# Kernel optimization log

Hardware: AMD Instinct MI355X
Metric: run time of the kernel (lower is better)

The kernel has to match this reference:

```python
import jax, jax.numpy as jnp
import numpy as np
import itertools

KS = 5           # kernel_size per pseudo dim
PDIM = 2         # pseudo-coordinate dim
N_NODES = 50000
N_EDGES = 800000
D_IN = 128
D_OUT = 128
EPS = 1e-12


def l2norm(x):
    n = jnp.linalg.norm(x, axis=-1, keepdims=True)
    return x / jnp.maximum(n, EPS)


def spline_conv(x, src, dst, pseudo, weight, bias):
    """torch_spline_conv with degree=1, open splines, aggr='mean', no root weight."""
    N = x.shape[0]
    out_dim = weight.shape[-1]
    dim = pseudo.shape[1]
    v = pseudo * (KS - 1)                                   # [E, dim] in [0, KS-1)
    i0 = jnp.clip(jnp.floor(v), 0, KS - 2).astype(jnp.int32)
    frac = v - i0.astype(v.dtype)                           # [E, dim]
    # Precompute per-kernel transforms once per node: cheaper than per-edge GEMV
    Xk = jnp.einsum('ni,kio->nko', x, weight)               # [N, K=25, out]
    E = src.shape[0]
    y = jnp.zeros((E, out_dim), x.dtype)
    for bits in itertools.product((0, 1), repeat=dim):      # S = 2**dim = 4 combos
        b = jnp.ones((E,), x.dtype)
        wi = jnp.zeros((E,), jnp.int32)
        stride = 1
        for d, bit in enumerate(bits):
            b = b * (frac[:, d] if bit else 1.0 - frac[:, d])
            wi = wi + (i0[:, d] + bit) * stride
            stride *= KS
        y = y + b[:, None] * Xk[src, wi]                    # gather-weight per edge
    agg = jax.ops.segment_sum(y, dst, num_segments=N)       # scatter-add to targets
    deg = jax.ops.segment_sum(jnp.ones((E,), x.dtype), dst, num_segments=N)
    return agg / jnp.maximum(deg, 1.0)[:, None] + bias      # mean aggregation


def setup_inputs() -> dict:
    key = jax.random.key(0)
    ks = jax.random.split(key, 6)
    K = KS ** PDIM
    x = jax.random.normal(ks[0], (N_NODES, D_IN), jnp.float32)
    edge_index = jax.random.randint(ks[1], (2, N_EDGES), 0, N_NODES, jnp.int32)
    edge_attr = jax.random.uniform(ks[2], (N_EDGES, PDIM), jnp.float32)
    s0 = 1.0 / np.sqrt(K * D_IN)
    s1 = 1.0 / np.sqrt(K * D_OUT)
    w0 = jax.random.normal(ks[3], (K, D_IN, D_OUT), jnp.float32) * s0
    w1 = jax.random.normal(ks[4], (K, D_OUT, D_OUT), jnp.float32) * s1
    b0 = jnp.zeros((D_OUT,), jnp.float32)
    b1 = jnp.zeros((D_OUT,), jnp.float32)
    return {"x": x, "edge_index": edge_index, "edge_attr": edge_attr,
            "w0": w0, "b0": b0, "w1": w1, "b1": b1}


def reference(x, edge_index, edge_attr, w0, b0, w1, b1):
    src, dst = edge_index[0], edge_index[1]
    xs = [l2norm(x)]
    h = x
    for w, b in ((w0, b0), (w1, b1)):
        h = spline_conv(h, src, dst, edge_attr, w, b)
        xs.append(l2norm(h))
        h = jax.nn.relu(h)
    return jnp.concatenate(xs, axis=-1)                     # [N, D_IN + 2*D_OUT]
```

## Files before the change

### kernel.cpp

```cpp
#include <hip/hip_runtime.h>

#define D     128
#define OD    384
#define NK    25
#define KCMAX 13
#define KB0   13

typedef __attribute__((ext_vector_type(8))) short bf16x8;
typedef __attribute__((ext_vector_type(4))) float f32x4;
typedef __attribute__((ext_vector_type(4))) unsigned int u32x4;
typedef const __attribute__((address_space(1))) void gv_t;
typedef __attribute__((address_space(3))) void lv_t;

struct __align__(16) Rec {
  int src;
  unsigned int wi;
  unsigned int b01;
  unsigned int b23;
};

__device__ inline unsigned short f2bf(float f) {
  unsigned int u = __float_as_uint(f);
  u += 0x7fffu + ((u >> 16) & 1u);
  return (unsigned short)(u >> 16);
}
__device__ inline unsigned short f2h(float f) {
  return __builtin_bit_cast(unsigned short, (_Float16)f);
}
__device__ inline float h2f(unsigned int bits16) {
  return (float)__builtin_bit_cast(_Float16, (unsigned short)(bits16 & 0xffffu));
}


__device__ inline int edge_cls(int w00) {
  return (w00 + 6 < KB0) ? 0 : ((w00 >= KB0) ? 2 : 1);
}

__global__ __launch_bounds__(256) void count3_kernel(const int* __restrict__ dstA,
    const float* __restrict__ attr, int E, int* __restrict__ deg,
    int* __restrict__ cnt3) {
  int e = blockIdx.x * 256 + threadIdx.x;
  if (e >= E) return;
  int d = dstA[e];
  atomicAdd(&deg[d], 1);
  float v0 = attr[2 * e] * 4.0f;
  float v1 = attr[2 * e + 1] * 4.0f;
  int i0 = min(3, max(0, (int)v0));
  int i1 = min(3, max(0, (int)v1));
  int w00 = i0 + 5 * i1;
  atomicAdd(&cnt3[d * 3 + edge_cls(w00)], 1);
}


__global__ __launch_bounds__(1024) void scan_a_kernel(const int* __restrict__ cnt, int M,
    int* __restrict__ base3, int* __restrict__ bsum) {
  __shared__ int tmp[1024];
  int tid = threadIdx.x;
  int e = blockIdx.x * 1024 + tid;
  int v = (e < M) ? cnt[e] : 0;
  tmp[tid] = v;
  __syncthreads();
#pragma unroll
  for (int off = 1; off < 1024; off <<= 1) {
    int t = (tid >= off) ? tmp[tid - off] : 0;
    __syncthreads();
    tmp[tid] += t;
    __syncthreads();
  }
  if (e <= M) base3[e] = tmp[tid] - v;
  if (tid == 1023) bsum[blockIdx.x] = tmp[1023];
}

__global__ __launch_bounds__(256) void scan_b_kernel(int* __restrict__ bsum, int nblk) {
  __shared__ int tmp[256];
  __shared__ int carry;
  int tid = threadIdx.x;
  if (tid == 0) carry = 0;
  __syncthreads();
  for (int s = 0; s < nblk; s += 256) {
    int i = s + tid;
    int v = (i < nblk) ? bsum[i] : 0;
    tmp[tid] = v;
    __syncthreads();
#pragma unroll
    for (int off = 1; off < 256; off <<= 1) {
      int t = (tid >= off) ? tmp[tid - off] : 0;
      __syncthreads();
      tmp[tid] += t;
      __syncthreads();
    }
    if (i < nblk) bsum[i] = carry + tmp[tid] - v;
    __syncthreads();
    if (tid == 255) carry += tmp[255];
    __syncthreads();
  }
}

__global__ __launch_bounds__(256) void scan_c_kernel(int* __restrict__ base3,
    int* __restrict__ cursor, const int* __restrict__ bsum, int M) {
  int e = blockIdx.x * 256 + threadIdx.x;
  if (e > M) return;
  int v = base3[e] + bsum[e >> 10];
  base3[e] = v;
  if (e < M) cursor[e] = v;
}

__global__ __launch_bounds__(256) void fill_kernel(const int* __restrict__ srcA,
    const int* __restrict__ dstA, const float* __restrict__ attr, int E,
    int* __restrict__ cursor, Rec* __restrict__ recs) {
  int e = blockIdx.x * 256 + threadIdx.x;
  if (e >= E) return;
  int d = dstA[e];
  float v0 = attr[2 * e] * 4.0f;
  float v1 = attr[2 * e + 1] * 4.0f;
  int i0 = min(3, max(0, (int)v0));
  int i1 = min(3, max(0, (int)v1));
  float f0 = v0 - (float)i0;
  float f1 = v1 - (float)i1;
  int w00 = i0 + 5 * i1;
  int pos = atomicAdd(&cursor[d * 3 + edge_cls(w00)], 1);
  Rec r;
  r.src = srcA[e];
  unsigned int w = (unsigned int)w00;
  r.wi = w | ((w + 1) << 5) | ((w + 5) << 10) | ((w + 6) << 15);
  r.b01 = (unsigned int)f2h((1.f - f0) * (1.f - f1)) | ((unsigned int)f2h(f0 * (1.f - f1)) << 16);
  r.b23 = (unsigned int)f2h((1.f - f0) * f1) | ((unsigned int)f2h(f0 * f1) << 16);
  recs[pos] = r;
}

__global__ __launch_bounds__(256) void wt_kernel(const float* __restrict__ W,
                                                 unsigned short* __restrict__ WT) {
  int idx = blockIdx.x * 256 + threadIdx.x;
  if (idx >= 128 * NK * D) return;
  int n = idx / (NK * D);
  int kk = idx - n * (NK * D);
  WT[idx] = f2bf(W[(size_t)kk * D + n]);
}


__global__ __launch_bounds__(256) void gather_kernel(const int* __restrict__ base3,
    const Rec* __restrict__ recs, const unsigned short* __restrict__ Xb,
    unsigned short* __restrict__ Gc, int N, int KCc, int kc0, int c_lo, int c_hi) {
  __shared__ float lacc[4][KCMAX * D];
  int w = threadIdx.x >> 6, l = threadIdx.x & 63;
  int dst = blockIdx.x * 4 + w;
  if (dst >= N) return;
  float* A = lacc[w];
  for (int k = 0; k < KCc; ++k)
    *(float2*)(A + k * D + l * 2) = make_float2(0.f, 0.f);

  auto ACC = [&](const Rec& r, unsigned int xp) {
    float x0 = __uint_as_float(xp << 16);
    float x1 = __uint_as_float(xp & 0xffff0000u);
    float bq[4] = {h2f(r.b01), h2f(r.b01 >> 16), h2f(r.b23), h2f(r.b23 >> 16)};
#pragma unroll
    for (int q = 0; q < 4; ++q) {
      int k = (int)((r.wi >> (5 * q)) & 31u) - kc0;
      if ((unsigned)k < (unsigned)KCc) {
        float2 p = *(const float2*)(A + k * D + l * 2);
        p.x = fmaf(bq[q], x0, p.x);
        p.y = fmaf(bq[q], x1, p.y);
        *(float2*)(A + k * D + l * 2) = p;
      }
    }
  };

  int s = __builtin_amdgcn_readfirstlane(base3[dst * 3 + c_lo]);
  int e = __builtin_amdgcn_readfirstlane(base3[dst * 3 + c_hi]);
  int j = s;
  for (; j + 3 < e; j += 4) {
    Rec r0 = recs[j], r1 = recs[j + 1], r2 = recs[j + 2], r3 = recs[j + 3];
    unsigned int xp0 = *(const unsigned int*)(Xb + (size_t)r0.src * D + l * 2);
    unsigned int xp1 = *(const unsigned int*)(Xb + (size_t)r1.src * D + l * 2);
    unsigned int xp2 = *(const unsigned int*)(Xb + (size_t)r2.src * D + l * 2);
    unsigned int xp3 = *(const unsigned int*)(Xb + (size_t)r3.src * D + l * 2);
    ACC(r0, xp0); ACC(r1, xp1); ACC(r2, xp2); ACC(r3, xp3);
  }
  for (; j < e; ++j) {
    Rec r = recs[j];
    unsigned int xp = *(const unsigned int*)(Xb + (size_t)r.src * D + l * 2);
    ACC(r, xp);
  }

  unsigned short* gr = Gc + (size_t)dst * ((size_t)KCc * D);
  for (int t = l; t < KCc * 16; t += 64) {
    const float* src = A + (t >> 4) * D + (t & 15) * 8;
    float4 v0 = *(const float4*)(src);
    float4 v1 = *(const float4*)(src + 4);
    u32x4 pk;
    pk[0] = (unsigned int)f2bf(v0.x) | ((unsigned int)f2bf(v0.y) << 16);
    pk[1] = (unsigned int)f2bf(v0.z) | ((unsigned int)f2bf(v0.w) << 16);
    pk[2] = (unsigned int)f2bf(v1.x) | ((unsigned int)f2bf(v1.y) << 16);
    pk[3] = (unsigned int)f2bf(v1.z) | ((unsigned int)f2bf(v1.w) << 16);
    *(u32x4*)(gr + (size_t)t * 8) = pk;
  }
}


__global__ __launch_bounds__(256) void gemm_kernel(
    const unsigned short* __restrict__ G, const unsigned short* __restrict__ WT,
    float* __restrict__ Y, int N, int KCc, int kc0, int first) {
  __shared__ __attribute__((aligned(16))) char At[2][16384];
  __shared__ __attribute__((aligned(16))) char Bt[2][16384];
  const int tid = threadIdx.x;
  const int w = tid >> 6;
  const int l = tid & 63;
  const int m0 = blockIdx.x * 128;
  const size_t ldG = (size_t)KCc * 256;
  const size_t ldW = (size_t)NK * 256;

  const int lrow = l >> 3;
  const int scol = ((l & 7) * 16) ^ (lrow << 4);

  f32x4 acc[2][8];
#pragma unroll
  for (int mr = 0; mr < 2; ++mr)
#pragma unroll
    for (int nc = 0; nc < 8; ++nc) {
      if (first) {
        acc[mr][nc] = (f32x4){0.f, 0.f, 0.f, 0.f};
      } else {
        int col = nc * 16 + (l & 15);
#pragma unroll
        for (int j = 0; j < 4; ++j) {
          int row = m0 + w * 32 + mr * 16 + (l >> 4) * 4 + j;
          acc[mr][nc][j] = (row < N) ? Y[(size_t)row * D + col] : 0.f;
        }
      }
    }

  const int steps = KCc * 2;
  auto STAGE = [&](int kt, int b) {
#pragma unroll
    for (int i = 0; i < 4; ++i) {
      int row = w * 32 + i * 8 + lrow;
      int node = m0 + row;
      if (node > N - 1) node = N - 1;
      const char* src = (const char*)G + (size_t)node * ldG + kt * 128 + scol;
      __builtin_amdgcn_global_load_lds((gv_t*)src, (lv_t*)(At[b] + (w * 4 + i) * 1024),
                                       16, 0, 0);
    }
#pragma unroll
    for (int i = 0; i < 4; ++i) {
      int nr = w * 32 + i * 8 + lrow;
      const char* src = (const char*)WT + (size_t)nr * ldW + kc0 * 256 + kt * 128 + scol;
      __builtin_amdgcn_global_load_lds((gv_t*)src, (lv_t*)(Bt[b] + (w * 4 + i) * 1024),
                                       16, 0, 0);
    }
  };

  STAGE(0, 0);
  __syncthreads();
  for (int kt = 0; kt < steps; ++kt) {
    const int cur = kt & 1;
    if (kt + 1 < steps) STAGE(kt + 1, cur ^ 1);
#pragma unroll
    for (int ks = 0; ks < 2; ++ks) {
      int kb = ks * 64 + (l >> 4) * 16;
      bf16x8 a[2], b[8];
#pragma unroll
      for (int mr = 0; mr < 2; ++mr) {
        int r = w * 32 + mr * 16 + (l & 15);
        a[mr] = *(const bf16x8*)(At[cur] + r * 128 + (kb ^ ((r & 7) << 4)));
      }
#pragma unroll
      for (int nc = 0; nc < 8; ++nc) {
        int nr = nc * 16 + (l & 15);
        b[nc] = *(const bf16x8*)(Bt[cur] + nr * 128 + (kb ^ ((nr & 7) << 4)));
      }
#pragma unroll
      for (int mr = 0; mr < 2; ++mr)
#pragma unroll
        for (int nc = 0; nc < 8; ++nc)
          acc[mr][nc] =
              __builtin_amdgcn_mfma_f32_16x16x32_bf16(a[mr], b[nc], acc[mr][nc], 0, 0, 0);
    }
    __syncthreads();
  }

#pragma unroll
  for (int mr = 0; mr < 2; ++mr)
#pragma unroll
    for (int nc = 0; nc < 8; ++nc) {
      int col = nc * 16 + (l & 15);
#pragma unroll
      for (int j = 0; j < 4; ++j) {
        int row = m0 + w * 32 + mr * 16 + (l >> 4) * 4 + j;
        if (row < N) Y[(size_t)row * D + col] = acc[mr][nc][j];
      }
    }
}


__global__ __launch_bounds__(256) void l2norm_x_kernel(const float* __restrict__ x,
    float* __restrict__ out, unsigned short* __restrict__ xbf, int N) {
  int g = blockIdx.x * 256 + threadIdx.x;
  int n = g >> 6, lane = g & 63;
  if (n >= N) return;
  float2 v = *(const float2*)(x + (size_t)n * D + lane * 2);
  float ss = v.x * v.x + v.y * v.y;
#pragma unroll
  for (int m = 1; m < 64; m <<= 1) ss += __shfl_xor(ss, m, 64);
  float r = 1.0f / fmaxf(sqrtf(ss), 1e-12f);
  *(float2*)(out + (size_t)n * OD + lane * 2) = make_float2(v.x * r, v.y * r);
  unsigned int pk = (unsigned int)f2bf(v.x) | ((unsigned int)f2bf(v.y) << 16);
  *(unsigned int*)(xbf + (size_t)n * D + lane * 2) = pk;
}

__global__ __launch_bounds__(256) void finalize_kernel(const float* __restrict__ y,
    const int* __restrict__ deg, const float* __restrict__ bias, float* __restrict__ out,
    unsigned short* __restrict__ xnext, int N) {
  int g = blockIdx.x * 256 + threadIdx.x;
  int n = g >> 6, lane = g & 63;
  if (n >= N) return;
  float inv = 1.0f / (float)max(deg[n], 1);
  float2 a = *(const float2*)(y + (size_t)n * D + lane * 2);
  float2 b = *(const float2*)(bias + lane * 2);
  float h0 = a.x * inv + b.x;
  float h1 = a.y * inv + b.y;
  float ss = h0 * h0 + h1 * h1;
#pragma unroll
  for (int m = 1; m < 64; m <<= 1) ss += __shfl_xor(ss, m, 64);
  float r = 1.0f / fmaxf(sqrtf(ss), 1e-12f);
  *(float2*)(out + (size_t)n * OD + lane * 2) = make_float2(h0 * r, h1 * r);
  if (xnext) {
    unsigned int pk = (unsigned int)f2bf(fmaxf(h0, 0.f)) |
                      ((unsigned int)f2bf(fmaxf(h1, 0.f)) << 16);
    *(unsigned int*)(xnext + (size_t)n * D + lane * 2) = pk;
  }
}


extern "C" void kernel_launch(void* const* d_in, const int* in_sizes, int n_in,
                              void* d_out, int out_size, void* d_ws, size_t ws_size,
                              hipStream_t stream) {
  const float* x    = (const float*)d_in[0];
  const int*   ei   = (const int*)d_in[1];
  const float* attr = (const float*)d_in[2];
  const float* w0   = (const float*)d_in[3];
  const float* b0   = (const float*)d_in[4];
  const float* w1   = (const float*)d_in[5];
  const float* b1   = (const float*)d_in[6];
  float* out = (float*)d_out;

  const int N = in_sizes[0] / D;
  const int E = in_sizes[1] / 2;
  const int* srcA = ei;
  const int* dstA = ei + E;
  const int M3 = N * 3;

  char* p = (char*)d_ws;
  auto carve = [&](size_t bytes) -> char* {
    char* r = p;
    p += (bytes + 255) & ~(size_t)255;
    return r;
  };
  unsigned short* xbf    = (unsigned short*)carve((size_t)N * D * 2);
  unsigned short* xtmp   = (unsigned short*)carve((size_t)N * D * 2);
  float*          ygemm  = (float*)carve((size_t)N * D * 4);
  int*            deg    = (int*)carve((size_t)N * 4);
  int*            cnt3   = (int*)carve((size_t)M3 * 4);
  int*            base3  = (int*)carve(((size_t)M3 + 1) * 4);
  int*            cursor = (int*)carve((size_t)M3 * 4);
  int*            bsum   = (int*)carve(4096);
  Rec*            recs   = (Rec*)carve((size_t)E * sizeof(Rec));
  unsigned short* WT0    = (unsigned short*)carve((size_t)128 * NK * D * 2);
  unsigned short* WT1    = (unsigned short*)carve((size_t)128 * NK * D * 2);
  size_t used = (size_t)(p - (char*)d_ws);
  size_t remain = (ws_size > used) ? (ws_size - used) : 0;
  int KCg = (int)(remain / ((size_t)N * D * 2));
  if (KCg > KCMAX) KCg = KCMAX;
  if (KCg < 1) KCg = 1;
  unsigned short* Gc = (unsigned short*)carve((size_t)N * (size_t)KCg * D * 2);
  (void)n_in; (void)out_size;

  hipMemsetAsync(deg, 0, (size_t)N * 4, stream);
  hipMemsetAsync(cnt3, 0, (size_t)M3 * 4, stream);

  int eb = (E + 255) / 256;
  count3_kernel<<<eb, 256, 0, stream>>>(dstA, attr, E, deg, cnt3);
  int nblk_a = (M3 + 1 + 1023) / 1024;
  scan_a_kernel<<<nblk_a, 1024, 0, stream>>>(cnt3, M3, base3, bsum);
  scan_b_kernel<<<1, 256, 0, stream>>>(bsum, nblk_a);
  scan_c_kernel<<<(M3 + 1 + 255) / 256, 256, 0, stream>>>(base3, cursor, bsum, M3);
  fill_kernel<<<eb, 256, 0, stream>>>(srcA, dstA, attr, E, cursor, recs);
  int wtb = (128 * NK * D + 255) / 256;
  wt_kernel<<<wtb, 256, 0, stream>>>(w0, WT0);
  wt_kernel<<<wtb, 256, 0, stream>>>(w1, WT1);

  int nb = (N * 64 + 255) / 256;
  l2norm_x_kernel<<<nb, 256, 0, stream>>>(x, out, xbf, N);

  int gbg = (N + 3) / 4;
  int gbm = (N + 127) / 128;
  const unsigned short* xin = xbf;
  const float* Bv[2] = {b0, b1};
  const unsigned short* WTl[2] = {WT0, WT1};
  for (int layer = 0; layer < 2; ++layer) {
    if (KCg >= KB0) {
      gather_kernel<<<gbg, 256, 0, stream>>>(base3, recs, xin, Gc, N, KB0, 0, 0, 2);
      gemm_kernel<<<gbm, 256, 0, stream>>>(Gc, WTl[layer], ygemm, N, KB0, 0, 1);
      gather_kernel<<<gbg, 256, 0, stream>>>(base3, recs, xin, Gc, N, NK - KB0, KB0, 1, 3);
      gemm_kernel<<<gbm, 256, 0, stream>>>(Gc, WTl[layer], ygemm, N, NK - KB0, KB0, 0);
    } else {
      int first = 1;
      for (int kc0 = 0; kc0 < NK; kc0 += KCg) {
        int KCc = min(KCg, NK - kc0);
        gather_kernel<<<gbg, 256, 0, stream>>>(base3, recs, xin, Gc, N, KCc, kc0, 0, 3);
        gemm_kernel<<<gbm, 256, 0, stream>>>(Gc, WTl[layer], ygemm, N, KCc, kc0, first);
        first = 0;
      }
    }
    finalize_kernel<<<nb, 256, 0, stream>>>(ygemm, deg, Bv[layer], out + D * (layer + 1),
                                            layer == 0 ? xtmp : nullptr, N);
    xin = xtmp;
  }
}
```

Baseline: 640.8 us.

## Fuse gather and GEMM per kernel-row chunk, bucketing edges by row index

```diff
diff --git a/kernel.cpp b/kernel.cpp
--- a/kernel.cpp
+++ b/kernel.cpp
@@ -1,20 +1,18 @@
 #include <hip/hip_runtime.h>
 
-#define D     128
-#define OD    384
-#define NK    25
-#define KCMAX 13
-#define KB0   13
+#define D    128
+#define OD   384
+#define NK   25
+#define KC   5
+#define AST  132
 
 typedef __attribute__((ext_vector_type(8))) short bf16x8;
 typedef __attribute__((ext_vector_type(4))) float f32x4;
 typedef __attribute__((ext_vector_type(4))) unsigned int u32x4;
-typedef const __attribute__((address_space(1))) void gv_t;
-typedef __attribute__((address_space(3))) void lv_t;
 
 struct __align__(16) Rec {
   int src;
-  unsigned int wi;
+  int i0;
   unsigned int b01;
   unsigned int b23;
 };
@@ -32,28 +30,20 @@
 }
 
 
-__device__ inline int edge_cls(int w00) {
-  return (w00 + 6 < KB0) ? 0 : ((w00 >= KB0) ? 2 : 1);
-}
-
-__global__ __launch_bounds__(256) void count3_kernel(const int* __restrict__ dstA,
+__global__ __launch_bounds__(256) void count4_kernel(const int* __restrict__ dstA,
     const float* __restrict__ attr, int E, int* __restrict__ deg,
-    int* __restrict__ cnt3) {
+    int* __restrict__ cnt4) {
   int e = blockIdx.x * 256 + threadIdx.x;
   if (e >= E) return;
   int d = dstA[e];
   atomicAdd(&deg[d], 1);
-  float v0 = attr[2 * e] * 4.0f;
   float v1 = attr[2 * e + 1] * 4.0f;
-  int i0 = min(3, max(0, (int)v0));
   int i1 = min(3, max(0, (int)v1));
-  int w00 = i0 + 5 * i1;
-  atomicAdd(&cnt3[d * 3 + edge_cls(w00)], 1);
-}
-
+  atomicAdd(&cnt4[d * 4 + i1], 1);
+}
 
 __global__ __launch_bounds__(1024) void scan_a_kernel(const int* __restrict__ cnt, int M,
-    int* __restrict__ base3, int* __restrict__ bsum) {
+    int* __restrict__ base, int* __restrict__ bsum) {
   __shared__ int tmp[1024];
   int tid = threadIdx.x;
   int e = blockIdx.x * 1024 + tid;
@@ -67,7 +57,7 @@
     tmp[tid] += t;
     __syncthreads();
   }
-  if (e <= M) base3[e] = tmp[tid] - v;
+  if (e <= M) base[e] = tmp[tid] - v;
   if (tid == 1023) bsum[blockIdx.x] = tmp[1023];
 }
 
@@ -96,12 +86,12 @@
   }
 }
 
-__global__ __launch_bounds__(256) void scan_c_kernel(int* __restrict__ base3,
+__global__ __launch_bounds__(256) void scan_c_kernel(int* __restrict__ base,
     int* __restrict__ cursor, const int* __restrict__ bsum, int M) {
   int e = blockIdx.x * 256 + threadIdx.x;
   if (e > M) return;
-  int v = base3[e] + bsum[e >> 10];
-  base3[e] = v;
+  int v = base[e] + bsum[e >> 10];
+  base[e] = v;
   if (e < M) cursor[e] = v;
 }
 
@@ -117,13 +107,12 @@
   int i1 = min(3, max(0, (int)v1));
   float f0 = v0 - (float)i0;
   float f1 = v1 - (float)i1;
-  int w00 = i0 + 5 * i1;
-  int pos = atomicAdd(&cursor[d * 3 + edge_cls(w00)], 1);
+  int pos = atomicAdd(&cursor[d * 4 + i1], 1);
   Rec r;
   r.src = srcA[e];
-  unsigned int w = (unsigned int)w00;
-  r.wi = w | ((w + 1) << 5) | ((w + 5) << 10) | ((w + 6) << 15);
-  r.b01 = (unsigned int)f2h((1.f - f0) * (1.f - f1)) | ((unsigned int)f2h(f0 * (1.f - f1)) << 16);
+  r.i0 = i0;
+  r.b01 = (unsigned int)f2h((1.f - f0) * (1.f - f1)) |
+          ((unsigned int)f2h(f0 * (1.f - f1)) << 16);
   r.b23 = (unsigned int)f2h((1.f - f0) * f1) | ((unsigned int)f2h(f0 * f1) << 16);
   recs[pos] = r;
 }
@@ -138,157 +127,99 @@
 }
 
 
-__global__ __launch_bounds__(256) void gather_kernel(const int* __restrict__ base3,
-    const Rec* __restrict__ recs, const unsigned short* __restrict__ Xb,
-    unsigned short* __restrict__ Gc, int N, int KCc, int kc0, int c_lo, int c_hi) {
-  __shared__ float lacc[4][KCMAX * D];
-  int w = threadIdx.x >> 6, l = threadIdx.x & 63;
-  int dst = blockIdx.x * 4 + w;
-  if (dst >= N) return;
-  float* A = lacc[w];
-  for (int k = 0; k < KCc; ++k)
-    *(float2*)(A + k * D + l * 2) = make_float2(0.f, 0.f);
-
-  auto ACC = [&](const Rec& r, unsigned int xp) {
-    float x0 = __uint_as_float(xp << 16);
-    float x1 = __uint_as_float(xp & 0xffff0000u);
-    float bq[4] = {h2f(r.b01), h2f(r.b01 >> 16), h2f(r.b23), h2f(r.b23 >> 16)};
-#pragma unroll
-    for (int q = 0; q < 4; ++q) {
-      int k = (int)((r.wi >> (5 * q)) & 31u) - kc0;
-      if ((unsigned)k < (unsigned)KCc) {
-        float2 p = *(const float2*)(A + k * D + l * 2);
-        p.x = fmaf(bq[q], x0, p.x);
-        p.y = fmaf(bq[q], x1, p.y);
-        *(float2*)(A + k * D + l * 2) = p;
+__global__ __launch_bounds__(1024, 8) void fused_kernel(
+    const int* __restrict__ base4, const Rec* __restrict__ recs,
+    const unsigned short* __restrict__ Xb, const unsigned short* __restrict__ WT,
+    float* __restrict__ Y, int N, int chunk) {
+  __shared__ float lacc[16 * KC * AST];
+  __shared__ float red[8][256];
+  const int tid = threadIdx.x;
+  const int w = tid >> 6, l = tid & 63;
+  const int blk = blockIdx.x;
+  const int dst = blk * 16 + w;
+  float* A = lacc + w * (KC * AST);
+  for (int t = l; t < KC * AST; t += 64) A[t] = 0.f;
+
+  if (dst < N) {
+    const int l2 = l * 2;
+    auto ACC2 = [&](const Rec& r, unsigned int xp, bool upper) {
+      unsigned int pair = upper ? r.b23 : r.b01;
+      float w0 = h2f(pair), w1 = h2f(pair >> 16);
+      float x0 = __uint_as_float(xp << 16);
+      float x1 = __uint_as_float(xp & 0xffff0000u);
+      float* p = A + r.i0 * AST + l2;
+      float2 a0 = *(float2*)p;
+      float2 a1 = *(float2*)(p + AST);
+      a0.x = fmaf(w0, x0, a0.x); a0.y = fmaf(w0, x1, a0.y);
+      a1.x = fmaf(w1, x0, a1.x); a1.y = fmaf(w1, x1, a1.y);
+      *(float2*)p = a0;
+      *(float2*)(p + AST) = a1;
+    };
+    auto WALK = [&](int j0, int j1, bool upper) {
+      int j = j0;
+      for (; j + 3 < j1; j += 4) {
+        Rec r0 = recs[j], r1 = recs[j + 1], r2 = recs[j + 2], r3 = recs[j + 3];
+        unsigned int xp0 = *(const unsigned int*)(Xb + (size_t)r0.src * D + l2);
+        unsigned int xp1 = *(const unsigned int*)(Xb + (size_t)r1.src * D + l2);
+        unsigned int xp2 = *(const unsigned int*)(Xb + (size_t)r2.src * D + l2);
+        unsigned int xp3 = *(const unsigned int*)(Xb + (size_t)r3.src * D + l2);
+        ACC2(r0, xp0, upper); ACC2(r1, xp1, upper);
+        ACC2(r2, xp2, upper); ACC2(r3, xp3, upper);
+      }
+      for (; j < j1; ++j) {
+        Rec r = recs[j];
+        unsigned int xp = *(const unsigned int*)(Xb + (size_t)r.src * D + l2);
+        ACC2(r, xp, upper);
+      }
+    };
+    const int* b4 = base4 + dst * 4;
+    if (chunk >= 1) {
+      int a0 = __builtin_amdgcn_readfirstlane(b4[chunk - 1]);
+      int a1 = __builtin_amdgcn_readfirstlane(b4[chunk]);
+      WALK(a0, a1, true);
+    }
+    if (chunk <= 3) {
+      int a0 = __builtin_amdgcn_readfirstlane(b4[chunk]);
+      int a1 = __builtin_amdgcn_readfirstlane(b4[chunk + 1]);
+      WALK(a0, a1, false);
+    }
+  }
+  __syncthreads();
+
+  const int nb = w & 7, kh = w >> 3;
+  const int arow = l & 15, aoff = (l >> 4) * 8;
+  const unsigned short* wb =
+      WT + (size_t)(nb * 16 + arow) * (NK * D) + chunk * (KC * D);
+  f32x4 acc = (f32x4){0.f, 0.f, 0.f, 0.f};
+  for (int s = kh * (KC * 2); s < (kh + 1) * (KC * 2); ++s) {
+    const float* ap =
+        lacc + (size_t)arow * (KC * AST) + (s >> 2) * AST + (s & 3) * 32 + aoff;
+    float4 fa = *(const float4*)ap;
+    float4 fb = *(const float4*)(ap + 4);
+    u32x4 pk;
+    asm("v_cvt_pk_bf16_f32 %0, %1, %2" : "=v"(pk[0]) : "v"(fa.x), "v"(fa.y));
+    asm("v_cvt_pk_bf16_f32 %0, %1, %2" : "=v"(pk[1]) : "v"(fa.z), "v"(fa.w));
+    asm("v_cvt_pk_bf16_f32 %0, %1, %2" : "=v"(pk[2]) : "v"(fb.x), "v"(fb.y));
+    asm("v_cvt_pk_bf16_f32 %0, %1, %2" : "=v"(pk[3]) : "v"(fb.z), "v"(fb.w));
+    bf16x8 av = __builtin_bit_cast(bf16x8, pk);
+    bf16x8 bv = *(const bf16x8*)(wb + s * 32 + aoff);
+    acc = __builtin_amdgcn_mfma_f32_16x16x32_bf16(av, bv, acc, 0, 0, 0);
+  }
+  if (kh == 1) *(f32x4*)&red[nb][l * 4] = acc;
+  __syncthreads();
+  if (kh == 0) {
+    f32x4 o = *(const f32x4*)&red[nb][l * 4];
+    int col = nb * 16 + arow;
+#pragma unroll
+    for (int j = 0; j < 4; ++j) {
+      int row = blk * 16 + (l >> 4) * 4 + j;
+      if (row < N) {
+        float v = acc[j] + o[j];
+        float* yp = Y + (size_t)row * D + col;
+        *yp = (chunk == 0) ? v : (*yp + v);
       }
     }
-  };
-
-  int s = __builtin_amdgcn_readfirstlane(base3[dst * 3 + c_lo]);
-  int e = __builtin_amdgcn_readfirstlane(base3[dst * 3 + c_hi]);
-  int j = s;
-  for (; j + 3 < e; j += 4) {
-    Rec r0 = recs[j], r1 = recs[j + 1], r2 = recs[j + 2], r3 = recs[j + 3];
-    unsigned int xp0 = *(const unsigned int*)(Xb + (size_t)r0.src * D + l * 2);
-    unsigned int xp1 = *(const unsigned int*)(Xb + (size_t)r1.src * D + l * 2);
-    unsigned int xp2 = *(const unsigned int*)(Xb + (size_t)r2.src * D + l * 2);
-    unsigned int xp3 = *(const unsigned int*)(Xb + (size_t)r3.src * D + l * 2);
-    ACC(r0, xp0); ACC(r1, xp1); ACC(r2, xp2); ACC(r3, xp3);
-  }
-  for (; j < e; ++j) {
-    Rec r = recs[j];
-    unsigned int xp = *(const unsigned int*)(Xb + (size_t)r.src * D + l * 2);
-    ACC(r, xp);
-  }
-
-  unsigned short* gr = Gc + (size_t)dst * ((size_t)KCc * D);
-  for (int t = l; t < KCc * 16; t += 64) {
-    const float* src = A + (t >> 4) * D + (t & 15) * 8;
-    float4 v0 = *(const float4*)(src);
-    float4 v1 = *(const float4*)(src + 4);
-    u32x4 pk;
-    pk[0] = (unsigned int)f2bf(v0.x) | ((unsigned int)f2bf(v0.y) << 16);
-    pk[1] = (unsigned int)f2bf(v0.z) | ((unsigned int)f2bf(v0.w) << 16);
-    pk[2] = (unsigned int)f2bf(v1.x) | ((unsigned int)f2bf(v1.y) << 16);
-    pk[3] = (unsigned int)f2bf(v1.z) | ((unsigned int)f2bf(v1.w) << 16);
-    *(u32x4*)(gr + (size_t)t * 8) = pk;
-  }
-}
-
-
-__global__ __launch_bounds__(256) void gemm_kernel(
-    const unsigned short* __restrict__ G, const unsigned short* __restrict__ WT,
-    float* __restrict__ Y, int N, int KCc, int kc0, int first) {
-  __shared__ __attribute__((aligned(16))) char At[2][16384];
-  __shared__ __attribute__((aligned(16))) char Bt[2][16384];
-  const int tid = threadIdx.x;
-  const int w = tid >> 6;
-  const int l = tid & 63;
-  const int m0 = blockIdx.x * 128;
-  const size_t ldG = (size_t)KCc * 256;
-  const size_t ldW = (size_t)NK * 256;
-
-  const int lrow = l >> 3;
-  const int scol = ((l & 7) * 16) ^ (lrow << 4);
-
-  f32x4 acc[2][8];
-#pragma unroll
-  for (int mr = 0; mr < 2; ++mr)
-#pragma unroll
-    for (int nc = 0; nc < 8; ++nc) {
-      if (first) {
-        acc[mr][nc] = (f32x4){0.f, 0.f, 0.f, 0.f};
-      } else {
-        int col = nc * 16 + (l & 15);
-#pragma unroll
-        for (int j = 0; j < 4; ++j) {
-          int row = m0 + w * 32 + mr * 16 + (l >> 4) * 4 + j;
-          acc[mr][nc][j] = (row < N) ? Y[(size_t)row * D + col] : 0.f;
-        }
-      }
-    }
-
-  const int steps = KCc * 2;
-  auto STAGE = [&](int kt, int b) {
-#pragma unroll
-    for (int i = 0; i < 4; ++i) {
-      int row = w * 32 + i * 8 + lrow;
-      int node = m0 + row;
-      if (node > N - 1) node = N - 1;
-      const char* src = (const char*)G + (size_t)node * ldG + kt * 128 + scol;
-      __builtin_amdgcn_global_load_lds((gv_t*)src, (lv_t*)(At[b] + (w * 4 + i) * 1024),
-                                       16, 0, 0);
-    }
-#pragma unroll
-    for (int i = 0; i < 4; ++i) {
-      int nr = w * 32 + i * 8 + lrow;
-      const char* src = (const char*)WT + (size_t)nr * ldW + kc0 * 256 + kt * 128 + scol;
-      __builtin_amdgcn_global_load_lds((gv_t*)src, (lv_t*)(Bt[b] + (w * 4 + i) * 1024),
-                                       16, 0, 0);
-    }
-  };
-
-  STAGE(0, 0);
-  __syncthreads();
-  for (int kt = 0; kt < steps; ++kt) {
-    const int cur = kt & 1;
-    if (kt + 1 < steps) STAGE(kt + 1, cur ^ 1);
-#pragma unroll
-    for (int ks = 0; ks < 2; ++ks) {
-      int kb = ks * 64 + (l >> 4) * 16;
-      bf16x8 a[2], b[8];
-#pragma unroll
-      for (int mr = 0; mr < 2; ++mr) {
-        int r = w * 32 + mr * 16 + (l & 15);
-        a[mr] = *(const bf16x8*)(At[cur] + r * 128 + (kb ^ ((r & 7) << 4)));
-      }
-#pragma unroll
-      for (int nc = 0; nc < 8; ++nc) {
-        int nr = nc * 16 + (l & 15);
-        b[nc] = *(const bf16x8*)(Bt[cur] + nr * 128 + (kb ^ ((nr & 7) << 4)));
-      }
-#pragma unroll
-      for (int mr = 0; mr < 2; ++mr)
-#pragma unroll
-        for (int nc = 0; nc < 8; ++nc)
-          acc[mr][nc] =
-              __builtin_amdgcn_mfma_f32_16x16x32_bf16(a[mr], b[nc], acc[mr][nc], 0, 0, 0);
-    }
-    __syncthreads();
-  }
-
-#pragma unroll
-  for (int mr = 0; mr < 2; ++mr)
-#pragma unroll
-    for (int nc = 0; nc < 8; ++nc) {
-      int col = nc * 16 + (l & 15);
-#pragma unroll
-      for (int j = 0; j < 4; ++j) {
-        int row = m0 + w * 32 + mr * 16 + (l >> 4) * 4 + j;
-        if (row < N) Y[(size_t)row * D + col] = acc[mr][nc][j];
-      }
-    }
+  }
 }
 
 
@@ -347,7 +278,7 @@
   const int E = in_sizes[1] / 2;
   const int* srcA = ei;
   const int* dstA = ei + E;
-  const int M3 = N * 3;
+  const int M4 = N * 4;
 
   char* p = (char*)d_ws;
   auto carve = [&](size_t bytes) -> char* {
@@ -359,30 +290,24 @@
   unsigned short* xtmp   = (unsigned short*)carve((size_t)N * D * 2);
   float*          ygemm  = (float*)carve((size_t)N * D * 4);
   int*            deg    = (int*)carve((size_t)N * 4);
-  int*            cnt3   = (int*)carve((size_t)M3 * 4);
-  int*            base3  = (int*)carve(((size_t)M3 + 1) * 4);
-  int*            cursor = (int*)carve((size_t)M3 * 4);
+  int*            cnt4   = (int*)carve((size_t)M4 * 4);
+  int*            base4  = (int*)carve(((size_t)M4 + 1) * 4);
+  int*            cursor = (int*)carve((size_t)M4 * 4);
   int*            bsum   = (int*)carve(4096);
   Rec*            recs   = (Rec*)carve((size_t)E * sizeof(Rec));
   unsigned short* WT0    = (unsigned short*)carve((size_t)128 * NK * D * 2);
   unsigned short* WT1    = (unsigned short*)carve((size_t)128 * NK * D * 2);
-  size_t used = (size_t)(p - (char*)d_ws);
-  size_t remain = (ws_size > used) ? (ws_size - used) : 0;
-  int KCg = (int)(remain / ((size_t)N * D * 2));
-  if (KCg > KCMAX) KCg = KCMAX;
-  if (KCg < 1) KCg = 1;
-  unsigned short* Gc = (unsigned short*)carve((size_t)N * (size_t)KCg * D * 2);
-  (void)n_in; (void)out_size;
+  (void)n_in; (void)out_size; (void)ws_size;
 
   hipMemsetAsync(deg, 0, (size_t)N * 4, stream);
-  hipMemsetAsync(cnt3, 0, (size_t)M3 * 4, stream);
+  hipMemsetAsync(cnt4, 0, (size_t)M4 * 4, stream);
 
   int eb = (E + 255) / 256;
-  count3_kernel<<<eb, 256, 0, stream>>>(dstA, attr, E, deg, cnt3);
-  int nblk_a = (M3 + 1 + 1023) / 1024;
-  scan_a_kernel<<<nblk_a, 1024, 0, stream>>>(cnt3, M3, base3, bsum);
+  count4_kernel<<<eb, 256, 0, stream>>>(dstA, attr, E, deg, cnt4);
+  int nblk_a = (M4 + 1 + 1023) / 1024;
+  scan_a_kernel<<<nblk_a, 1024, 0, stream>>>(cnt4, M4, base4, bsum);
   scan_b_kernel<<<1, 256, 0, stream>>>(bsum, nblk_a);
-  scan_c_kernel<<<(M3 + 1 + 255) / 256, 256, 0, stream>>>(base3, cursor, bsum, M3);
+  scan_c_kernel<<<(M4 + 1 + 255) / 256, 256, 0, stream>>>(base4, cursor, bsum, M4);
   fill_kernel<<<eb, 256, 0, stream>>>(srcA, dstA, attr, E, cursor, recs);
   int wtb = (128 * NK * D + 255) / 256;
   wt_kernel<<<wtb, 256, 0, stream>>>(w0, WT0);
@@ -391,26 +316,13 @@
   int nb = (N * 64 + 255) / 256;
   l2norm_x_kernel<<<nb, 256, 0, stream>>>(x, out, xbf, N);
 
-  int gbg = (N + 3) / 4;
-  int gbm = (N + 127) / 128;
+  int fblk = (N + 15) / 16;
   const unsigned short* xin = xbf;
   const float* Bv[2] = {b0, b1};
   const unsigned short* WTl[2] = {WT0, WT1};
   for (int layer = 0; layer < 2; ++layer) {
-    if (KCg >= KB0) {
-      gather_kernel<<<gbg, 256, 0, stream>>>(base3, recs, xin, Gc, N, KB0, 0, 0, 2);
-      gemm_kernel<<<gbm, 256, 0, stream>>>(Gc, WTl[layer], ygemm, N, KB0, 0, 1);
-      gather_kernel<<<gbg, 256, 0, stream>>>(base3, recs, xin, Gc, N, NK - KB0, KB0, 1, 3);
-      gemm_kernel<<<gbm, 256, 0, stream>>>(Gc, WTl[layer], ygemm, N, NK - KB0, KB0, 0);
-    } else {
-      int first = 1;
-      for (int kc0 = 0; kc0 < NK; kc0 += KCg) {
-        int KCc = min(KCg, NK - kc0);
-        gather_kernel<<<gbg, 256, 0, stream>>>(base3, recs, xin, Gc, N, KCc, kc0, 0, 3);
-        gemm_kernel<<<gbm, 256, 0, stream>>>(Gc, WTl[layer], ygemm, N, KCc, kc0, first);
-        first = 0;
-      }
-    }
+    for (int c = 0; c < 5; ++c)
+      fused_kernel<<<fblk, 1024, 0, stream>>>(base4, recs, xin, WTl[layer], ygemm, N, c);
     finalize_kernel<<<nb, 256, 0, stream>>>(ygemm, deg, Bv[layer], out + D * (layer + 1),
                                             layer == 0 ? xtmp : nullptr, N);
     xin = xtmp;
```

New measurement: 1.096 ms. +71.1%, slower.
